# Kernel tuning notes

Hardware: AMD Instinct MI355X
Metric: run time of the kernel (lower is better)

## Reference

```python
import jax, jax.numpy as jnp
import numpy as np

EPS_SK = 1e-8   # Sinkhorn epsilon
EPS_LN = 1e-5   # torch LayerNorm default eps
N_ITER = 20


def _layer_norm(x, eps=EPS_LN):
    mu = jnp.mean(x, axis=-1, keepdims=True)
    var = jnp.mean((x - mu) ** 2, axis=-1, keepdims=True)
    return (x - mu) * jax.lax.rsqrt(var + eps)


def _sinkhorn(H):
    M = jnp.exp(H)
    def body(_, M):
        M = M / (jnp.sum(M, axis=-1, keepdims=True) + EPS_SK)
        M = M / (jnp.sum(M, axis=-2, keepdims=True) + EPS_SK)
        return M
    return jax.lax.fori_loop(0, N_ITER, body, M)


def setup_inputs() -> dict:
    key = jax.random.key(0)
    ks = jax.random.split(key, 12)
    B, S, D = 8192, 4, 1024
    sc_in = 1.0 / np.sqrt(S * D)
    sc_d = 1.0 / np.sqrt(D)
    return {
        "x": jax.random.normal(ks[0], (B, D), jnp.float32),
        "x_streams": jax.random.normal(ks[1], (B, S, D), jnp.float32),
        "W_pre": jax.random.normal(ks[2], (S, S * D), jnp.float32) * sc_in,
        "b_pre": jnp.zeros((S,), jnp.float32),
        "W_post": jax.random.normal(ks[3], (S, S * D), jnp.float32) * sc_in,
        "b_post": jnp.zeros((S,), jnp.float32),
        "W_res": jax.random.normal(ks[4], (S * S, S * D), jnp.float32) * sc_in,
        "b_res": jnp.zeros((S * S,), jnp.float32),
        "alpha_pre": jnp.float32(0.01),
        "alpha_post": jnp.float32(0.01),
        "alpha_res": jnp.float32(0.01),
        "gamma": jnp.ones((D,), jnp.float32),
        "beta": jnp.zeros((D,), jnp.float32),
        "W_layer": jax.random.normal(ks[5], (D, D), jnp.float32) * sc_d,
        "b_layer": jnp.zeros((D,), jnp.float32),
    }


def reference(x, x_streams, W_pre, b_pre, W_post, b_post, W_res, b_res,
              alpha_pre, alpha_post, alpha_res, gamma, beta, W_layer, b_layer):
    B = x.shape[0]
    S = x_streams.shape[1]
    x_flat = x_streams.reshape(B, -1)            # [B, S*D]
    x_norm = _layer_norm(x_flat)                 # F.layer_norm, no affine

    h_pre = jax.nn.sigmoid(alpha_pre * (x_norm @ W_pre.T + b_pre))   # [B, S]
    x_agg = jnp.einsum('bs,bsd->bd', h_pre, x_streams)               # [B, D]

    # layer_fn modeled as a Linear (self.norm has affine gamma/beta)
    out = (_layer_norm(x_agg) * gamma + beta) @ W_layer.T + b_layer  # [B, D]

    h_post = 2.0 * jax.nn.sigmoid(alpha_post * (x_norm @ W_post.T + b_post))  # [B, S]
    h_res_logits = alpha_res * (x_norm @ W_res.T + b_res)                      # [B, S*S]
    h_res = _sinkhorn(h_res_logits.reshape(B, S, S))                           # [B, S, S]

    mixed = jnp.einsum('bst,btd->bsd', h_res, x_streams)             # [B, S, D]
    updated = mixed + out[:, None, :] * h_post[:, :, None]
    return (jnp.mean(updated, axis=1), updated)
```

## Files before the change

### kernel.cpp

```cpp
#include <hip/hip_runtime.h>

#define DEV __device__ __forceinline__

typedef __bf16 bf16x8 __attribute__((ext_vector_type(8)));
typedef float f32x4 __attribute__((ext_vector_type(4)));
typedef unsigned int u32;

constexpr int BROWS = 8192;
constexpr int D = 1024;
constexpr int SD = 4096;

DEV unsigned short f2bf(float f) {
  unsigned int u = __float_as_uint(f);
  u = (u + 0x7FFFu + ((u >> 16) & 1u)) >> 16;
  return (unsigned short)u;
}

DEV float wred(float v) {
#pragma unroll
  for (int m = 1; m < 64; m <<= 1) v += __shfl_xor(v, m);
  return v;
}

DEV float sigmoidf(float x) { return 1.0f / (1.0f + __expf(-x)); }

DEV void async_ld16(const void* g, void* l) {
  __builtin_amdgcn_global_load_lds((const __attribute__((address_space(1))) u32*)g,
                                   (__attribute__((address_space(3))) u32*)l, 16, 0, 0);
}

__global__ __launch_bounds__(256) void k0_prep(
    const float* __restrict__ Wlayer, const float* __restrict__ Wpre,
    const float* __restrict__ Wpost, const float* __restrict__ Wres,
    unsigned short* __restrict__ wl16, float* __restrict__ Wall,
    float* __restrict__ wsum) {
  const int bx = blockIdx.x, tid = threadIdx.x;
  if (bx < 1024) {
    const int i = bx * 1024 + tid * 4;
    float4 v = *(const float4*)(Wlayer + i);
    ushort4 u = make_ushort4(f2bf(v.x), f2bf(v.y), f2bf(v.z), f2bf(v.w));
    *(ushort4*)(wl16 + i) = u;
  } else {
    const int j = bx - 1024;
    const float* src = (j < 4) ? (Wpre + j * SD)
                               : (j < 8 ? (Wpost + (j - 4) * SD) : (Wres + (j - 8) * SD));
    float s = 0.f;
    for (int i = tid * 4; i < SD; i += 1024) {
      float4 v = *(const float4*)(src + i);
      *(float4*)(Wall + j * SD + i) = v;
      s += v.x + v.y + v.z + v.w;
    }
    s = wred(s);
    __shared__ float tmp[4];
    if ((tid & 63) == 0) tmp[tid >> 6] = s;
    __syncthreads();
    if (tid == 0) wsum[j] = tmp[0] + tmp[1] + tmp[2] + tmp[3];
  }
}

__global__ __launch_bounds__(256) void k1_rowpass(
    const float* __restrict__ xs, const float* __restrict__ Wall,
    const float* __restrict__ bpre, const float* __restrict__ bpost,
    const float* __restrict__ bres,
    const float* __restrict__ s_apre, const float* __restrict__ s_apost,
    const float* __restrict__ s_ares,
    const float* __restrict__ gamma, const float* __restrict__ beta,
    const float* __restrict__ wsum,
    unsigned short* __restrict__ lnagg,
    float* __restrict__ hres_g, float* __restrict__ hpost_g) {
  const int tid = threadIdx.x;
  const int wv = tid >> 6;
  const int ln = tid & 63;
  const int rb = blockIdx.x * 4;

  __shared__ float DOT[24][4];
  __shared__ float HPRE[4][4];

  const int jb = wv * 6;
  const float* Wb = Wall + (size_t)jb * SD;
  const float* xb0 = xs + (size_t)rb * SD;
  const int l4 = ln * 4;

  float acc6[6][4];
#pragma unroll
  for (int q = 0; q < 6; ++q)
#pragma unroll
    for (int r = 0; r < 4; ++r) acc6[q][r] = 0.f;
  float sum4[4] = {0.f, 0.f, 0.f, 0.f}, sq4[4] = {0.f, 0.f, 0.f, 0.f};

  float4 xA[4], wA[6], xB[4], wB[6];

#define LDX(dst, it)                                      \
  {                                                       \
    const int i_ = (it)*256 + l4;                         \
    dst[0] = *(const float4*)(xb0 + i_);                  \
    dst[1] = *(const float4*)(xb0 + SD + i_);             \
    dst[2] = *(const float4*)(xb0 + 2 * SD + i_);         \
    dst[3] = *(const float4*)(xb0 + 3 * SD + i_);         \
  }
#define LDW(dst, it)                                      \
  {                                                       \
    const int i_ = (it)*256 + l4;                         \
    _Pragma("unroll") for (int q = 0; q < 6; ++q)         \
        dst[q] = *(const float4*)(Wb + q * SD + i_);      \
  }
#define CMP(X, W)                                                              \
  {                                                                            \
    _Pragma("unroll") for (int r = 0; r < 4; ++r) {                            \
      sum4[r] += X[r].x + X[r].y + X[r].z + X[r].w;                            \
      sq4[r] += X[r].x * X[r].x + X[r].y * X[r].y + X[r].z * X[r].z +          \
                X[r].w * X[r].w;                                               \
    }                                                                          \
    _Pragma("unroll") for (int q = 0; q < 6; ++q) {                            \
      _Pragma("unroll") for (int r = 0; r < 4; ++r) acc6[q][r] +=              \
          W[q].x * X[r].x + W[q].y * X[r].y + W[q].z * X[r].z + W[q].w * X[r].w;\
    }                                                                          \
  }

  LDX(xA, 0);
  LDW(wA, 0);
#pragma unroll 1
  for (int it = 0; it < 16; it += 2) {
    LDX(xB, it + 1);
    LDW(wB, it + 1);
    CMP(xA, wA);
    if (it < 14) {
      LDX(xA, it + 2);
      LDW(wA, it + 2);
    }
    CMP(xB, wB);
  }
#undef LDX
#undef LDW
#undef CMP

#pragma unroll
  for (int q = 0; q < 6; ++q)
#pragma unroll
    for (int r = 0; r < 4; ++r) acc6[q][r] = wred(acc6[q][r]);
#pragma unroll
  for (int r = 0; r < 4; ++r) { sum4[r] = wred(sum4[r]); sq4[r] = wred(sq4[r]); }

  float mu4[4], rs4[4];
#pragma unroll
  for (int r = 0; r < 4; ++r) {
    mu4[r] = sum4[r] * (1.0f / 4096.0f);
    rs4[r] = rsqrtf(sq4[r] * (1.0f / 4096.0f) - mu4[r] * mu4[r] + 1e-5f);
  }

  if (ln == 0) {
#pragma unroll
    for (int q = 0; q < 6; ++q)
#pragma unroll
      for (int r = 0; r < 4; ++r) DOT[jb + q][r] = acc6[q][r];
  }
  __syncthreads();

  if (wv == 0) {
    const float ares = s_ares[0];
    const int rr = ln >> 4, jj = ln & 15;
    const float corr = rs4[rr] * (DOT[8 + jj][rr] - mu4[rr] * wsum[8 + jj]);
    float M = __expf(ares * (corr + bres[jj]));
#pragma unroll 1
    for (int itr = 0; itr < 20; ++itr) {
      float rs = M + __shfl_xor(M, 1);
      rs += __shfl_xor(rs, 2);
      M *= __builtin_amdgcn_rcpf(rs + 1e-8f);
      float cs = M + __shfl_xor(M, 4);
      cs += __shfl_xor(cs, 8);
      M *= __builtin_amdgcn_rcpf(cs + 1e-8f);
    }
    hres_g[(size_t)rb * 16 + ln] = M;
  } else if (wv == 1) {
    if (ln < 16) {
      const int r = ln >> 2, s = ln & 3;
      const float corr = rs4[r] * (DOT[s][r] - mu4[r] * wsum[s]);
      HPRE[r][s] = sigmoidf(s_apre[0] * (corr + bpre[s]));
    } else if (ln < 32) {
      const int idx = ln - 16, r = idx >> 2, s = idx & 3;
      const float corr = rs4[r] * (DOT[4 + s][r] - mu4[r] * wsum[4 + s]);
      hpost_g[(rb + r) * 4 + s] = 2.0f * sigmoidf(s_apost[0] * (corr + bpost[s]));
    }
  }
  __syncthreads();

  {
    const int b = rb + wv;
    const float* xb = xs + (size_t)b * SD;
    const float h0 = HPRE[wv][0], h1 = HPRE[wv][1], h2 = HPRE[wv][2], h3 = HPRE[wv][3];
    float4 agg[4];
    float asum = 0.f, asq = 0.f;
#pragma unroll
    for (int i2 = 0; i2 < 4; ++i2) {
      const int d = i2 * 256 + l4;
      float4 g0 = *(const float4*)(xb + d);
      float4 g1 = *(const float4*)(xb + D + d);
      float4 g2 = *(const float4*)(xb + 2 * D + d);
      float4 g3 = *(const float4*)(xb + 3 * D + d);
      float4 a;
      a.x = h0 * g0.x + h1 * g1.x + h2 * g2.x + h3 * g3.x;
      a.y = h0 * g0.y + h1 * g1.y + h2 * g2.y + h3 * g3.y;
      a.z = h0 * g0.z + h1 * g1.z + h2 * g2.z + h3 * g3.z;
      a.w = h0 * g0.w + h1 * g1.w + h2 * g2.w + h3 * g3.w;
      agg[i2] = a;
      asum += a.x + a.y + a.z + a.w;
      asq += a.x * a.x + a.y * a.y + a.z * a.z + a.w * a.w;
    }
    asum = wred(asum);
    asq = wred(asq);
    const float mu2 = asum * (1.0f / 1024.0f);
    const float rstd2 = rsqrtf(asq * (1.0f / 1024.0f) - mu2 * mu2 + 1e-5f);
#pragma unroll
    for (int i2 = 0; i2 < 4; ++i2) {
      const int d = i2 * 256 + l4;
      float4 g = *(const float4*)(gamma + d);
      float4 bb = *(const float4*)(beta + d);
      ushort4 u;
      u.x = f2bf((agg[i2].x - mu2) * rstd2 * g.x + bb.x);
      u.y = f2bf((agg[i2].y - mu2) * rstd2 * g.y + bb.y);
      u.z = f2bf((agg[i2].z - mu2) * rstd2 * g.z + bb.z);
      u.w = f2bf((agg[i2].w - mu2) * rstd2 * g.w + bb.w);
      *(ushort4*)(lnagg + (size_t)b * D + d) = u;
    }
  }
}

__global__ __launch_bounds__(256) void k2_gemm_ep(
    const unsigned short* __restrict__ A,
    const unsigned short* __restrict__ Bw,
    const float* __restrict__ blayer,
    const float* __restrict__ xs,
    const float* __restrict__ hres_g, const float* __restrict__ hpost_g,
    float* __restrict__ outMean, float* __restrict__ outUpd) {
  __shared__ char smem[44032];
  char* AsB = smem;
  char* BsB = smem + 16384;
  float* EP = (float*)smem;
  float* HR = (float*)(smem + 32768);
  float* HP = (float*)(smem + 41472);

  const int tid = threadIdx.x;
  const int l = tid & 63;
  const int wv = tid >> 6;
  const int wm = wv >> 1, wn = wv & 1;
  const int lrow = l & 15, lq = l >> 4;
  const int bm0 = blockIdx.x * 128;
  const int bn0 = blockIdx.y * 128;

#pragma unroll
  for (int i = 0; i < 8; ++i) {
    int idx = i * 256 + tid;
    HR[(idx >> 4) * 17 + (idx & 15)] = hres_g[(size_t)bm0 * 16 + idx];
  }
#pragma unroll
  for (int i = 0; i < 2; ++i) {
    int idx = i * 256 + tid;
    HP[(idx >> 2) * 5 + (idx & 3)] = hpost_g[(size_t)bm0 * 4 + idx];
  }

  f32x4 acc[4][4] = {};

#pragma unroll 1
  for (int kt = 0; kt < 16; ++kt) {
    __syncthreads();
#pragma unroll
    for (int c = 0; c < 4; ++c) {
      const int idx = c * 256 + tid;
      const int row = idx >> 3, cc = idx & 7;
      const int gch = cc ^ (row & 7);
      async_ld16((const char*)A + ((size_t)(bm0 + row) << 11) + kt * 128 + gch * 16,
                 AsB + idx * 16);
      async_ld16((const char*)Bw + ((size_t)(bn0 + row) << 11) + kt * 128 + gch * 16,
                 BsB + idx * 16);
    }
    __syncthreads();
#pragma unroll
    for (int kk = 0; kk < 2; ++kk) {
      bf16x8 af[4], bfr[4];
      const int sw = (kk * 4 + lq);
#pragma unroll
      for (int t = 0; t < 4; ++t) {
        const int ra = wm * 64 + t * 16 + lrow;
        const int rbr = wn * 64 + t * 16 + lrow;
        af[t] = *(const bf16x8*)(AsB + ra * 128 + (sw ^ (ra & 7)) * 16);
        bfr[t] = *(const bf16x8*)(BsB + rbr * 128 + (sw ^ (rbr & 7)) * 16);
      }
#pragma unroll
      for (int ti = 0; ti < 4; ++ti)
#pragma unroll
        for (int tj = 0; tj < 4; ++tj)
          acc[ti][tj] =
              __builtin_amdgcn_mfma_f32_16x16x32_bf16(af[ti], bfr[tj], acc[ti][tj], 0, 0, 0);
    }
  }

#pragma unroll
  for (int ti = 0; ti < 4; ++ti) {
    __syncthreads();
#pragma unroll
    for (int tj = 0; tj < 4; ++tj)
#pragma unroll
      for (int r2 = 0; r2 < 4; ++r2)
        EP[(wm * 16 + lq * 4 + r2) * 132 + wn * 64 + tj * 16 + lrow] = acc[ti][tj][r2];
    __syncthreads();

    const int rr2 = tid >> 3;
    const int c0 = (tid & 7) * 4;
    const int bl = (rr2 >> 4) * 64 + ti * 16 + (rr2 & 15);
    const int gr = bm0 + bl;
    float hr[16], hp4[4];
#pragma unroll
    for (int q = 0; q < 16; ++q) hr[q] = HR[bl * 17 + q];
#pragma unroll
    for (int q = 0; q < 4; ++q) hp4[q] = HP[bl * 5 + q];
    const float cm0 = 0.25f * (hr[0] + hr[4] + hr[8] + hr[12]);
    const float cm1 = 0.25f * (hr[1] + hr[5] + hr[9] + hr[13]);
    const float cm2 = 0.25f * (hr[2] + hr[6] + hr[10] + hr[14]);
    const float cm3 = 0.25f * (hr[3] + hr[7] + hr[11] + hr[15]);
    const float hps = 0.25f * (hp4[0] + hp4[1] + hp4[2] + hp4[3]);
    const float* xb = xs + (size_t)gr * SD + bn0;
    float* um = outMean + (size_t)gr * 1024 + bn0;
    float* uu = outUpd + (size_t)gr * 4096 + bn0;
#pragma unroll
    for (int k2i = 0; k2i < 4; ++k2i) {
      const int col = c0 + k2i * 32;
      f32x4 ov = *(const f32x4*)(EP + rr2 * 132 + col);
      ov += *(const f32x4*)(blayer + bn0 + col);
      const f32x4 x0 = *(const f32x4*)(xb + col);
      const f32x4 x1 = *(const f32x4*)(xb + 1024 + col);
      const f32x4 x2 = *(const f32x4*)(xb + 2048 + col);
      const f32x4 x3 = *(const f32x4*)(xb + 3072 + col);
      __builtin_nontemporal_store(cm0 * x0 + cm1 * x1 + cm2 * x2 + cm3 * x3 + ov * hps,
                                  (f32x4*)(um + col));
      __builtin_nontemporal_store(hr[0] * x0 + hr[1] * x1 + hr[2] * x2 + hr[3] * x3 + ov * hp4[0],
                                  (f32x4*)(uu + col));
      __builtin_nontemporal_store(hr[4] * x0 + hr[5] * x1 + hr[6] * x2 + hr[7] * x3 + ov * hp4[1],
                                  (f32x4*)(uu + 1024 + col));
      __builtin_nontemporal_store(hr[8] * x0 + hr[9] * x1 + hr[10] * x2 + hr[11] * x3 + ov * hp4[2],
                                  (f32x4*)(uu + 2048 + col));
      __builtin_nontemporal_store(hr[12] * x0 + hr[13] * x1 + hr[14] * x2 + hr[15] * x3 + ov * hp4[3],
                                  (f32x4*)(uu + 3072 + col));
    }
  }
}

extern "C" void kernel_launch(void* const* d_in, const int* in_sizes, int n_in,
                              void* d_out, int out_size, void* d_ws, size_t ws_size,
                              hipStream_t stream) {
  const float* xs = (const float*)d_in[1];
  const float* Wpre = (const float*)d_in[2];
  const float* bpre = (const float*)d_in[3];
  const float* Wpost = (const float*)d_in[4];
  const float* bpost = (const float*)d_in[5];
  const float* Wres = (const float*)d_in[6];
  const float* bres = (const float*)d_in[7];
  const float* apre = (const float*)d_in[8];
  const float* apost = (const float*)d_in[9];
  const float* ares = (const float*)d_in[10];
  const float* gamma = (const float*)d_in[11];
  const float* beta = (const float*)d_in[12];
  const float* Wlayer = (const float*)d_in[13];
  const float* blayer = (const float*)d_in[14];

  const size_t OFF_LNAGG = (size_t)2 << 20;
  const size_t OFF_HRES = (size_t)18 << 20;
  const size_t OFF_HPOST = OFF_HRES + (size_t)BROWS * 16 * 4;
  const size_t OFF_WSUM = OFF_HPOST + (size_t)BROWS * 4 * 4;
  const size_t OFF_WALL = OFF_WSUM + 512;
  const size_t NEED = OFF_WALL + (size_t)24 * SD * 4;
  if (ws_size < NEED) return;

  char* ws = (char*)d_ws;
  unsigned short* wl16 = (unsigned short*)ws;
  unsigned short* lnagg = (unsigned short*)(ws + OFF_LNAGG);
  float* hresb = (float*)(ws + OFF_HRES);
  float* hpostb = (float*)(ws + OFF_HPOST);
  float* wsum = (float*)(ws + OFF_WSUM);
  float* Wall = (float*)(ws + OFF_WALL);

  float* outMean = (float*)d_out;
  float* outUpd = outMean + (size_t)BROWS * D;

  hipLaunchKernelGGL(k0_prep, dim3(1048), dim3(256), 0, stream, Wlayer, Wpre, Wpost, Wres,
                     wl16, Wall, wsum);
  hipLaunchKernelGGL(k1_rowpass, dim3(2048), dim3(256), 0, stream, xs, Wall, bpre, bpost,
                     bres, apre, apost, ares, gamma, beta, wsum, lnagg, hresb, hpostb);
  hipLaunchKernelGGL(k2_gemm_ep, dim3(64, 8), dim3(256), 0, stream, lnagg, wl16, blayer, xs,
                     hresb, hpostb, outMean, outUpd);
}
```

Baseline: 396.7 us.

## Process eight rows per block in k1 with async LDS staging of x

The row-pass kernel now handles 8 batch rows per block instead of 4, so each loaded projection-weight vector is reused across twice as many rows and the weight traffic from L2 is roughly halved. Activation rows are copied asynchronously into a 4-deep LDS ring buffer, with explicit waitcnt/barrier steps inside an unrolled pipeline that overlaps weight and activation loads with the dot products. The Sinkhorn and sigmoid heads are spread across more waves. In exchange it uses more registers and LDS, adds a barrier per k-step, and launches half as many blocks.

Result: slower. 669.4 us (+68.7%).

```diff
diff --git a/kernel.cpp b/kernel.cpp
--- a/kernel.cpp
+++ b/kernel.cpp
@@ -58,7 +58,7 @@
   }
 }
 
-__global__ __launch_bounds__(256) void k1_rowpass(
+__global__ __launch_bounds__(256, 3) void k1_rowpass(
     const float* __restrict__ xs, const float* __restrict__ Wall,
     const float* __restrict__ bpre, const float* __restrict__ bpost,
     const float* __restrict__ bres,
@@ -71,123 +71,148 @@
   const int tid = threadIdx.x;
   const int wv = tid >> 6;
   const int ln = tid & 63;
-  const int rb = blockIdx.x * 4;
-
-  __shared__ float DOT[24][4];
-  __shared__ float HPRE[4][4];
+  const int rb = blockIdx.x * 8;
+  const int l4 = ln * 4;
+
+  __shared__ float XR[4][8][256];
+  __shared__ float DOT[24][8];
+  __shared__ float MU[8];
+  __shared__ float RSH[8];
+  __shared__ float HPRE[8][4];
 
   const int jb = wv * 6;
   const float* Wb = Wall + (size_t)jb * SD;
-  const float* xb0 = xs + (size_t)rb * SD;
-  const int l4 = ln * 4;
-
-  float acc6[6][4];
+  const float* gA = xs + (size_t)(rb + wv) * SD + l4;
+  const float* gB = xs + (size_t)(rb + 4 + wv) * SD + l4;
+
+  float acc[6][8];
 #pragma unroll
   for (int q = 0; q < 6; ++q)
 #pragma unroll
-    for (int r = 0; r < 4; ++r) acc6[q][r] = 0.f;
-  float sum4[4] = {0.f, 0.f, 0.f, 0.f}, sq4[4] = {0.f, 0.f, 0.f, 0.f};
-
-  float4 xA[4], wA[6], xB[4], wB[6];
-
-#define LDX(dst, it)                                      \
-  {                                                       \
-    const int i_ = (it)*256 + l4;                         \
-    dst[0] = *(const float4*)(xb0 + i_);                  \
-    dst[1] = *(const float4*)(xb0 + SD + i_);             \
-    dst[2] = *(const float4*)(xb0 + 2 * SD + i_);         \
-    dst[3] = *(const float4*)(xb0 + 3 * SD + i_);         \
-  }
-#define LDW(dst, it)                                      \
-  {                                                       \
-    const int i_ = (it)*256 + l4;                         \
-    _Pragma("unroll") for (int q = 0; q < 6; ++q)         \
-        dst[q] = *(const float4*)(Wb + q * SD + i_);      \
-  }
-#define CMP(X, W)                                                              \
-  {                                                                            \
-    _Pragma("unroll") for (int r = 0; r < 4; ++r) {                            \
-      sum4[r] += X[r].x + X[r].y + X[r].z + X[r].w;                            \
-      sq4[r] += X[r].x * X[r].x + X[r].y * X[r].y + X[r].z * X[r].z +          \
-                X[r].w * X[r].w;                                               \
-    }                                                                          \
-    _Pragma("unroll") for (int q = 0; q < 6; ++q) {                            \
-      _Pragma("unroll") for (int r = 0; r < 4; ++r) acc6[q][r] +=              \
-          W[q].x * X[r].x + W[q].y * X[r].y + W[q].z * X[r].z + W[q].w * X[r].w;\
-    }                                                                          \
-  }
-
-  LDX(xA, 0);
-  LDW(wA, 0);
-#pragma unroll 1
-  for (int it = 0; it < 16; it += 2) {
-    LDX(xB, it + 1);
-    LDW(wB, it + 1);
-    CMP(xA, wA);
-    if (it < 14) {
-      LDX(xA, it + 2);
-      LDW(wA, it + 2);
-    }
-    CMP(xB, wB);
-  }
-#undef LDX
+    for (int r = 0; r < 8; ++r) acc[q][r] = 0.f;
+  float s2a = 0.f, q2a = 0.f;
+  float s2b = 0.f, q2b = 0.f;
+
+  float4 wbufA[6], wbufB[6];
+
+#define LDW(dst, it)                                                      \
+  {                                                                       \
+    const float* p_ = Wb + (it) * 256 + l4;                               \
+    _Pragma("unroll") for (int q = 0; q < 6; ++q) dst[q] =                \
+        *(const float4*)(p_ + (size_t)q * SD);                            \
+  }
+#define DMA2(it)                                                          \
+  {                                                                       \
+    float* d_ = &XR[(it) & 3][0][0] + tid * 4;                            \
+    async_ld16(gA + (it) * 256, d_);                                      \
+    async_ld16(gB + (it) * 256, d_ + 1024);                               \
+  }
+#define CMP(it, W)                                                        \
+  {                                                                       \
+    const float* xb_ = &XR[(it) & 3][0][0] + l4;                          \
+    float4 xv[8];                                                         \
+    _Pragma("unroll") for (int r = 0; r < 8; ++r) xv[r] =                 \
+        *(const float4*)(xb_ + r * 256);                                  \
+    float4 sA_ = *(const float4*)(xb_ + wv * 256);                        \
+    float4 sB_ = *(const float4*)(xb_ + (4 + wv) * 256);                  \
+    s2a += sA_.x + sA_.y + sA_.z + sA_.w;                                 \
+    q2a += sA_.x * sA_.x + sA_.y * sA_.y + sA_.z * sA_.z + sA_.w * sA_.w; \
+    s2b += sB_.x + sB_.y + sB_.z + sB_.w;                                 \
+    q2b += sB_.x * sB_.x + sB_.y * sB_.y + sB_.z * sB_.z + sB_.w * sB_.w; \
+    _Pragma("unroll") for (int q = 0; q < 6; ++q) {                       \
+      _Pragma("unroll") for (int r = 0; r < 8; ++r) acc[q][r] +=          \
+          W[q].x * xv[r].x + W[q].y * xv[r].y + W[q].z * xv[r].z +        \
+          W[q].w * xv[r].w;                                               \
+    }                                                                     \
+  }
+#define KSTEP(I, WCUR, WNXT, LIT, DOW, DODMA)                             \
+  {                                                                       \
+    if (DOW) LDW(WNXT, (I) + 1);                                          \
+    if (DODMA) DMA2((I) + 2);                                             \
+    asm volatile("s_waitcnt vmcnt(" LIT ") lgkmcnt(0)" ::: "memory");     \
+    __builtin_amdgcn_s_barrier();                                         \
+    asm volatile("" ::: "memory");                                        \
+    CMP(I, WCUR);                                                         \
+  }
+
+  LDW(wbufA, 0);
+  DMA2(0);
+  DMA2(1);
+
+  KSTEP(0, wbufA, wbufB, "8", 1, 1)
+#pragma unroll
+  for (int i = 1; i <= 12; i += 2) {
+    KSTEP(i, wbufB, wbufA, "16", 1, 1)
+    KSTEP(i + 1, wbufA, wbufB, "16", 1, 1)
+  }
+  KSTEP(13, wbufB, wbufA, "16", 1, 1)
+  KSTEP(14, wbufA, wbufB, "14", 1, 0)
+  KSTEP(15, wbufB, wbufA, "6", 0, 0)
+#undef KSTEP
+#undef CMP
+#undef DMA2
 #undef LDW
-#undef CMP
 
 #pragma unroll
   for (int q = 0; q < 6; ++q)
 #pragma unroll
-    for (int r = 0; r < 4; ++r) acc6[q][r] = wred(acc6[q][r]);
-#pragma unroll
-  for (int r = 0; r < 4; ++r) { sum4[r] = wred(sum4[r]); sq4[r] = wred(sq4[r]); }
-
-  float mu4[4], rs4[4];
-#pragma unroll
-  for (int r = 0; r < 4; ++r) {
-    mu4[r] = sum4[r] * (1.0f / 4096.0f);
-    rs4[r] = rsqrtf(sq4[r] * (1.0f / 4096.0f) - mu4[r] * mu4[r] + 1e-5f);
-  }
+    for (int r = 0; r < 8; ++r) acc[q][r] = wred(acc[q][r]);
+  s2a = wred(s2a);
+  q2a = wred(q2a);
+  s2b = wred(s2b);
+  q2b = wred(q2b);
 
   if (ln == 0) {
 #pragma unroll
     for (int q = 0; q < 6; ++q)
 #pragma unroll
-      for (int r = 0; r < 4; ++r) DOT[jb + q][r] = acc6[q][r];
+      for (int r = 0; r < 8; ++r) DOT[jb + q][r] = acc[q][r];
+    const float mua = s2a * (1.0f / 4096.0f);
+    MU[wv] = mua;
+    RSH[wv] = rsqrtf(q2a * (1.0f / 4096.0f) - mua * mua + 1e-5f);
+    const float mub = s2b * (1.0f / 4096.0f);
+    MU[4 + wv] = mub;
+    RSH[4 + wv] = rsqrtf(q2b * (1.0f / 4096.0f) - mub * mub + 1e-5f);
   }
   __syncthreads();
 
-  if (wv == 0) {
+  if (wv < 2) {
     const float ares = s_ares[0];
-    const int rr = ln >> 4, jj = ln & 15;
-    const float corr = rs4[rr] * (DOT[8 + jj][rr] - mu4[rr] * wsum[8 + jj]);
+    const int rr = (wv << 2) + (ln >> 4), jj = ln & 15;
+    const float corr = RSH[rr] * (DOT[8 + jj][rr] - MU[rr] * wsum[8 + jj]);
     float M = __expf(ares * (corr + bres[jj]));
 #pragma unroll 1
     for (int itr = 0; itr < 20; ++itr) {
-      float rs = M + __shfl_xor(M, 1);
-      rs += __shfl_xor(rs, 2);
-      M *= __builtin_amdgcn_rcpf(rs + 1e-8f);
+      float rs_ = M + __shfl_xor(M, 1);
+      rs_ += __shfl_xor(rs_, 2);
+      M *= __builtin_amdgcn_rcpf(rs_ + 1e-8f);
       float cs = M + __shfl_xor(M, 4);
       cs += __shfl_xor(cs, 8);
       M *= __builtin_amdgcn_rcpf(cs + 1e-8f);
     }
-    hres_g[(size_t)rb * 16 + ln] = M;
-  } else if (wv == 1) {
-    if (ln < 16) {
+    hres_g[(size_t)(rb + rr) * 16 + jj] = M;
+  } else if (wv == 2) {
+    if (ln < 32) {
       const int r = ln >> 2, s = ln & 3;
-      const float corr = rs4[r] * (DOT[s][r] - mu4[r] * wsum[s]);
+      const float corr = RSH[r] * (DOT[s][r] - MU[r] * wsum[s]);
       HPRE[r][s] = sigmoidf(s_apre[0] * (corr + bpre[s]));
-    } else if (ln < 32) {
-      const int idx = ln - 16, r = idx >> 2, s = idx & 3;
-      const float corr = rs4[r] * (DOT[4 + s][r] - mu4[r] * wsum[4 + s]);
-      hpost_g[(rb + r) * 4 + s] = 2.0f * sigmoidf(s_apost[0] * (corr + bpost[s]));
+    }
+  } else {
+    if (ln < 32) {
+      const int r = ln >> 2, s = ln & 3;
+      const float corr = RSH[r] * (DOT[4 + s][r] - MU[r] * wsum[4 + s]);
+      hpost_g[(size_t)(rb + r) * 4 + s] = 2.0f * sigmoidf(s_apost[0] * (corr + bpost[s]));
     }
   }
   __syncthreads();
 
-  {
-    const int b = rb + wv;
+#pragma unroll
+  for (int rr2 = 0; rr2 < 2; ++rr2) {
+    const int hrow = wv * 2 + rr2;
+    const int b = rb + hrow;
     const float* xb = xs + (size_t)b * SD;
-    const float h0 = HPRE[wv][0], h1 = HPRE[wv][1], h2 = HPRE[wv][2], h3 = HPRE[wv][3];
+    const float h0 = HPRE[hrow][0], h1 = HPRE[hrow][1], h2 = HPRE[hrow][2],
+                h3 = HPRE[hrow][3];
     float4 agg[4];
     float asum = 0.f, asq = 0.f;
 #pragma unroll
@@ -383,7 +408,7 @@
 
   hipLaunchKernelGGL(k0_prep, dim3(1048), dim3(256), 0, stream, Wlayer, Wpre, Wpost, Wres,
                      wl16, Wall, wsum);
-  hipLaunchKernelGGL(k1_rowpass, dim3(2048), dim3(256), 0, stream, xs, Wall, bpre, bpost,
+  hipLaunchKernelGGL(k1_rowpass, dim3(1024), dim3(256), 0, stream, xs, Wall, bpre, bpost,
                      bres, apre, apost, ares, gamma, beta, wsum, lnagg, hresb, hpostb);
   hipLaunchKernelGGL(k2_gemm_ep, dim3(64, 8), dim3(256), 0, stream, lnagg, wl16, blayer, xs,
                      hresb, hpostb, outMean, outUpd);
```
